# Performance work log

Hardware: AMD Instinct MI355X
Metric: run time of the kernel (lower is better)

## Reference

```python
import jax, jax.numpy as jnp
import numpy as np

EMBED_DIM = 1024
BATCH = 4
SEQ = 2048


def setup_inputs() -> dict:
    key = jax.random.key(0)
    ks = jax.random.split(key, 9)
    D = EMBED_DIM
    s = 1.0 / np.sqrt(D)
    inputs = jax.random.normal(ks[0], (BATCH, SEQ, D), dtype=jnp.float32)
    rotation_params = jax.random.normal(ks[1], (D, D), dtype=jnp.float32) * s
    entangle_params = jax.random.normal(ks[2], (D, D), dtype=jnp.float32) * s
    Wq = jax.random.normal(ks[3], (D, D), dtype=jnp.float32) * s
    bq = jax.random.normal(ks[4], (D,), dtype=jnp.float32) * 0.01
    Wk = jax.random.normal(ks[5], (D, D), dtype=jnp.float32) * s
    bk = jax.random.normal(ks[6], (D,), dtype=jnp.float32) * 0.01
    Wv = jax.random.normal(ks[7], (D, D), dtype=jnp.float32) * s
    bv = jax.random.normal(ks[8], (D,), dtype=jnp.float32) * 0.01
    # causal mask: True = masked out (matches torch masked_fill semantics)
    mask = jnp.triu(jnp.ones((SEQ, SEQ), dtype=bool), k=1)
    return {"inputs": inputs, "rotation_params": rotation_params,
            "entangle_params": entangle_params, "Wq": Wq, "bq": bq,
            "Wk": Wk, "bk": bk, "Wv": Wv, "bv": bv, "mask": mask}


def reference(inputs, rotation_params, entangle_params, Wq, bq, Wk, bk, Wv, bv, mask):
    D = inputs.shape[-1]
    # q = Linear(x) @ R^T ; k = Linear(x) @ E^T ; v = Linear(x)
    q = (jnp.einsum('bsd,ed->bse', inputs, Wq) + bq) @ rotation_params.T
    k = (jnp.einsum('bsd,ed->bse', inputs, Wk) + bk) @ entangle_params.T
    v = jnp.einsum('bsd,ed->bse', inputs, Wv) + bv
    scores = jnp.einsum('bqd,bkd->bqk', q, k) / jnp.sqrt(jnp.float32(D))
    scores = jnp.where(mask, jnp.float32(-jnp.inf), scores)
    probs = jax.nn.softmax(scores, axis=-1)  # dropout=0.0 -> identity
    return jnp.einsum('bqk,bkd->bqd', probs, v)
```

## Files before the change

### kernel.cpp

```cpp
#include <hip/hip_runtime.h>
#include <hip/hip_bf16.h>
#include <stdint.h>
#include <math.h>

#define DD 1024
#define SS 2048
#define BB 4

typedef __bf16 bf16;
typedef __bf16 bf16x8 __attribute__((ext_vector_type(8)));
typedef __bf16 bf16x4 __attribute__((ext_vector_type(4)));
typedef float f32x4 __attribute__((ext_vector_type(4)));

__device__ __forceinline__ void gload_lds16(const bf16* g, bf16* l) {
  __builtin_amdgcn_global_load_lds(
      (const __attribute__((address_space(1))) void*)g,
      (__attribute__((address_space(3))) void*)l, 16, 0, 0);
}

__global__ __launch_bounds__(256) void prep_all(
    const float* __restrict__ x, const float* __restrict__ R,
    const float* __restrict__ E, const float* __restrict__ Wv,
    const float* __restrict__ Wq, const float* __restrict__ Wk,
    const float* __restrict__ bq, const float* __restrict__ bk,
    const float* __restrict__ bv, bf16* __restrict__ xb,
    bf16* __restrict__ Rb, bf16* __restrict__ Eb, bf16* __restrict__ Wvb,
    bf16* __restrict__ WqT, bf16* __restrict__ WkT, float* __restrict__ bias,
    float* __restrict__ rowsums) {
  int bid = blockIdx.x;
  int t = threadIdx.x;
  if (bid < 11264) {
    const float* src;
    bf16* dst;
    int base;
    if (bid < 8192) { src = x; dst = xb; base = bid; }
    else if (bid < 9216) { src = R; dst = Rb; base = bid - 8192; }
    else if (bid < 10240) { src = E; dst = Eb; base = bid - 9216; }
    else { src = Wv; dst = Wvb; base = bid - 10240; }
    int i = (base * 256 + t) * 4;
    float4 v = *(const float4*)(src + i);
    bf16x4 o;
    o.x = (bf16)v.x; o.y = (bf16)v.y; o.z = (bf16)v.z; o.w = (bf16)v.w;
    *(bf16x4*)(dst + i) = o;
  } else if (bid < 13312) {
    int r2 = bid - 11264;
    const float* src = (r2 >= 1024) ? Wk : Wq;
    bf16* dst = (r2 >= 1024) ? WkT : WqT;
    int rem = r2 & 1023;
    int bx = rem & 31, by = rem >> 5;
    __shared__ float tile[32][33];
    int tx = t & 31, ty = t >> 5;
    int xcol = bx * 32 + tx;
    int y0 = by * 32;
    for (int r = ty; r < 32; r += 8)
      tile[r][tx] = src[(y0 + r) * DD + xcol];
    __syncthreads();
    int dx = by * 32 + tx;
    int dy0 = bx * 32;
    for (int r = ty; r < 32; r += 8)
      dst[(dy0 + r) * DD + dx] = (bf16)tile[tx][r];
  } else if (bid < 16384) {
    int e = bid - 13312;
    if (e >= 2048) { if (t == 0) bias[e] = bv[e - 2048]; return; }
    const float* M = (e < 1024) ? R : E;
    const float* bb = (e < 1024) ? bq : bk;
    int row = e & 1023;
    float s = 0.f;
    for (int f = t; f < DD; f += 256) s += M[row * DD + f] * bb[f];
    for (int o = 32; o >= 1; o >>= 1) s += __shfl_xor(s, o, 64);
    __shared__ float red[4];
    if ((t & 63) == 0) red[t >> 6] = s;
    __syncthreads();
    if (t == 0) bias[e] = red[0] + red[1] + red[2] + red[3];
  } else {
    int idx = (bid - 16384) * 256 + t;
    rowsums[idx] = 0.f;
  }
}

#define STGA(p, h, kt)                                                       \
  gload_lds16(A + (long)((h) * 128 + w * 16 + srow) * DD + (kt) * 32 + scg,  \
              As + (p) * 8192 + (h) * 4096 + w * 512)
#define STGB(p, h, kt)                                                       \
  gload_lds16(B + (long)((h) * 128 + w * 16 + srow) * DD + (kt) * 32 + scg,  \
              Bs + (p) * 8192 + (h) * 4096 + w * 512)

#define PHASE(p, q, WAITN, ...)                                              \
  {                                                                          \
    bf16x8 af[4];                                                            \
    _Pragma("unroll") for (int i_ = 0; i_ < 4; i_++)                         \
        af[i_] = *(const bf16x8*)(a_base + (p) * 8192 + (q) * 2048 +         \
                                  i_ * 512);                                 \
    if ((q) == 0) {                                                          \
      _Pragma("unroll") for (int j_ = 0; j_ < 4; j_++)                       \
          bfr[j_] = *(const bf16x8*)(b_base + (p) * 8192 + j_ * 512);        \
    }                                                                        \
    __VA_ARGS__;                                                             \
    __builtin_amdgcn_s_barrier();                                            \
    asm volatile("s_waitcnt lgkmcnt(0)" ::: "memory");                       \
    __builtin_amdgcn_sched_barrier(0);                                       \
    __builtin_amdgcn_s_setprio(1);                                           \
    _Pragma("unroll") for (int i_ = 0; i_ < 4; i_++)                         \
        _Pragma("unroll") for (int j_ = 0; j_ < 4; j_++) acc[(q)*4 + i_][j_] \
        = __builtin_amdgcn_mfma_f32_16x16x32_bf16(af[i_], bfr[j_],           \
                                                  acc[(q)*4 + i_][j_], 0, 0, \
                                                  0);                        \
    __builtin_amdgcn_s_setprio(0);                                           \
    __builtin_amdgcn_sched_barrier(0);                                       \
    if ((WAITN) == 2) asm volatile("s_waitcnt vmcnt(2)" ::: "memory");       \
    if ((WAITN) == 0) asm volatile("s_waitcnt vmcnt(0)" ::: "memory");       \
    __builtin_amdgcn_s_barrier();                                            \
    __builtin_amdgcn_sched_barrier(0);                                       \
  }

__global__ __launch_bounds__(512, 2) void gemm256_qkv(
    const bf16* __restrict__ Ag, const bf16* __restrict__ Bg,
    bf16* __restrict__ Cg, const float* __restrict__ bias,
    bf16* __restrict__ vTp) {
  __shared__ __align__(16) bf16 smem[32768];
  bf16* As = smem;
  bf16* Bs = smem + 16384;

  int id = (int)blockIdx.y * 12 + (int)blockIdx.x;
  int wg = (id & 7) * 48 + (id >> 3);
  int bx = wg % 12, by = wg / 12;
  long m0 = (long)by * 256, n0 = (long)bx * 256;
  const bf16* A = Ag + m0 * DD;
  const bf16* B = Bg + n0 * DD;

  int t = threadIdx.x;
  int w = t >> 6, l = t & 63;
  int wm = w >> 2, wn = w & 3;
  int ln = l & 15, quad = l >> 4;

  int srow = l >> 2;
  int scg = ((l & 3) ^ ((l >> 3) & 3)) * 8;
  int rdslot = (quad ^ ((ln >> 1) & 3)) * 8;
  const bf16* a_base = As + (wm * 128 + ln) * 32 + rdslot;
  const bf16* b_base = Bs + (wn * 64 + ln) * 32 + rdslot;

  f32x4 acc[8][4];
#pragma unroll
  for (int i = 0; i < 8; i++)
#pragma unroll
    for (int j = 0; j < 4; j++) acc[i][j] = f32x4{0.f, 0.f, 0.f, 0.f};
  bf16x8 bfr[4];

  STGA(0, 0, 0); STGA(0, 1, 0);
  STGB(0, 0, 0); STGB(0, 1, 0);
  STGB(1, 0, 1); STGB(1, 1, 1);
  asm volatile("s_waitcnt vmcnt(2)" ::: "memory");
  __builtin_amdgcn_s_barrier();
  __builtin_amdgcn_sched_barrier(0);

#pragma unroll 1
  for (int t2 = 0; t2 < 30; t2 += 2) {
    PHASE(0, 0, -1, { STGA(1, 0, t2 + 1); STGA(1, 1, t2 + 1); })
    PHASE(0, 1, 2, { STGB(0, 0, t2 + 2); STGB(0, 1, t2 + 2); })
    PHASE(1, 0, -1, { STGA(0, 0, t2 + 2); STGA(0, 1, t2 + 2); })
    PHASE(1, 1, 2, { STGB(1, 0, t2 + 3); STGB(1, 1, t2 + 3); })
  }
  PHASE(0, 0, -1, { STGA(1, 0, 31); STGA(1, 1, 31); })
  PHASE(0, 1, 0, {})
  PHASE(1, 0, -1, {})
  PHASE(1, 1, -1, {})

  if (n0 < 2048) {
    bf16* C = Cg + m0 * 3072 + n0;
#pragma unroll
    for (int mf = 0; mf < 8; mf++) {
      int rb = wm * 128 + mf * 16 + quad * 4;
#pragma unroll
      for (int nf = 0; nf < 4; nf++) {
        int col = wn * 64 + nf * 16 + ln;
        float bv_ = bias[n0 + col];
#pragma unroll
        for (int r = 0; r < 4; r++)
          C[(long)(rb + r) * 3072 + col] = (bf16)(acc[mf][nf][r] + bv_);
      }
    }
  } else {
    int d0 = (int)n0 - 2048;
    int b = (int)(m0 >> 11);
    int s0 = (int)(m0 & 2047);
    for (int h = 0; h < 2; ++h) {
      __syncthreads();
      if (wm == h) {
#pragma unroll
        for (int mf = 0; mf < 8; mf++) {
          int sl = mf * 16 + quad * 4;
#pragma unroll
          for (int nf = 0; nf < 4; nf++) {
            int d = wn * 64 + nf * 16 + ln;
            float bv_ = bias[n0 + d];
#pragma unroll
            for (int r = 0; r < 4; r++)
              smem[d * 128 + ((sl + r) ^ ((d & 7) << 3))] =
                  (bf16)(acc[mf][nf][r] + bv_);
          }
        }
      }
      __syncthreads();
      int d = t >> 1, sh = t & 1;
      bf16* dst = vTp + (long)b * DD * SS + (long)(d0 + d) * SS + s0 +
                  h * 128 + sh * 64;
#pragma unroll
      for (int c = 0; c < 8; ++c) {
        int sc = (sh * 64 + c * 8) ^ ((d & 7) << 3);
        *(bf16x8*)(dst + c * 8) = *(const bf16x8*)(smem + d * 128 + sc);
      }
    }
  }
}

template <int MODE>
__global__ __launch_bounds__(256, 4)
void gemm_bt(const bf16* __restrict__ Ag, long lda, long sAb,
             const bf16* __restrict__ Bg, long ldb, long sBb,
             void* __restrict__ Cg, long ldc, long sCb,
             const float* __restrict__ bias, float scale, int K,
             bf16* __restrict__ vTp, float* __restrict__ rowsums) {
  __shared__ __align__(16) bf16 smem[16384];
  bf16* As = smem;
  bf16* Bs = smem + 8192;

  int bx = blockIdx.x, by = blockIdx.y, bz = blockIdx.z;
  if (MODE == 0 || MODE == 1) {
    int nx = (int)gridDim.x;
    int nwg = nx * (int)gridDim.y;
    int id = by * nx + bx;
    int xcd = id & 7, rest = id >> 3;
    int q8 = nwg >> 3, r8 = nwg & 7;
    int wg = (xcd < r8 ? xcd * (q8 + 1) : r8 * (q8 + 1) + (xcd - r8) * q8)
             + rest;
    bx = wg % nx;
    by = wg / nx;
  }
  if (MODE == 1) {
    int q = bx;
    by = (int)((sqrtf(8.f * q + 1.f) - 1.f) * 0.5f);
    while ((by + 1) * (by + 2) / 2 <= q) by++;
    while (by * (by + 1) / 2 > q) by--;
    bx = q - by * (by + 1) / 2;
  }
  if (MODE == 2) by = 15 - by;
  long m0 = (long)by * 128, n0 = (long)bx * 128;
  const bf16* A = Ag + (long)bz * sAb + m0 * lda;
  const bf16* Bp = Bg + (long)bz * sBb + n0 * ldb;

  int t = threadIdx.x;
  int w = t >> 6, l = t & 63;
  int lr = l >> 2;
  int lc = (((l & 3) ^ (lr & 3)) * 8);
  int quad = l >> 4, ln = l & 15;
  int wm = w >> 1, wn = w & 1;
  int rdoff = ((quad ^ (ln & 3)) * 8);

  int Keff = (MODE == 2) ? (by + 1) * 128 : K;

  f32x4 acc[4][4];
#pragma unroll
  for (int i = 0; i < 4; i++)
#pragma unroll
    for (int j = 0; j < 4; j++) acc[i][j] = f32x4{0.f, 0.f, 0.f, 0.f};

  const bf16* a_base = As + (wm * 64 + ln) * 32 + rdoff;
  const bf16* b_base = Bs + (wn * 64 + ln) * 32 + rdoff;
  long arow0 = (long)(w * 16 + lr);

#define STG(p, kc0)                                                         \
  {                                                                         \
    int kc = (kc0) + lc;                                                    \
    gload_lds16(A + arow0 * lda + kc, As + (p) * 4096 + w * 512);           \
    gload_lds16(A + (arow0 + 64) * lda + kc,                                \
                As + (p) * 4096 + 2048 + w * 512);                          \
    gload_lds16(Bp + arow0 * ldb + kc, Bs + (p) * 4096 + w * 512);          \
    gload_lds16(Bp + (arow0 + 64) * ldb + kc,                               \
                Bs + (p) * 4096 + 2048 + w * 512);                          \
  }

  STG(0, 0);
  int cur = 0;
  for (int k = 0; k < Keff; k += 32) {
    asm volatile("s_waitcnt vmcnt(0)" ::: "memory");
    __builtin_amdgcn_s_barrier();
    __builtin_amdgcn_sched_barrier(0);
    if (k + 32 < Keff) STG(cur ^ 1, k + 32);
    bf16x8 af[4], bfr[4];
#pragma unroll
    for (int i = 0; i < 4; i++) {
      af[i] = *(const bf16x8*)(a_base + cur * 4096 + i * 512);
      bfr[i] = *(const bf16x8*)(b_base + cur * 4096 + i * 512);
    }
#pragma unroll
    for (int i = 0; i < 4; i++)
#pragma unroll
      for (int j = 0; j < 4; j++)
        acc[i][j] = __builtin_amdgcn_mfma_f32_16x16x32_bf16(
            af[i], bfr[j], acc[i][j], 0, 0, 0);
    cur ^= 1;
  }
#undef STG
  __syncthreads();

  if (MODE == 0) {
    bf16* C = (bf16*)Cg + (long)bz * sCb + m0 * ldc + n0;
#pragma unroll
    for (int i = 0; i < 4; i++) {
      int rb = wm * 64 + i * 16 + quad * 4;
#pragma unroll
      for (int j = 0; j < 4; j++) {
        int col = wn * 64 + j * 16 + ln;
        float bv_ = bias ? bias[n0 + col] : 0.f;
#pragma unroll
        for (int r = 0; r < 4; r++)
          C[(long)(rb + r) * ldc + col] = (bf16)(acc[i][j][r] + bv_);
      }
    }
  } else if (MODE == 1) {
#pragma unroll
    for (int i = 0; i < 4; i++) {
      int rb = wm * 64 + i * 16 + quad * 4;
#pragma unroll
      for (int j = 0; j < 4; j++) {
        int col = wn * 64 + j * 16 + ln;
#pragma unroll
        for (int r = 0; r < 4; r++) {
          int row = rb + r;
          float p = 0.f;
          if (n0 + col <= m0 + row) p = __expf(acc[i][j][r] * scale);
          smem[row * 128 + (col ^ ((row & 15) << 3))] = (bf16)p;
        }
      }
    }
    __syncthreads();
    int row = t >> 1, h = t & 1;
    bf16* P = (bf16*)Cg + (long)bz * sCb + (m0 + row) * ldc + n0;
    float rsum = 0.f;
#pragma unroll
    for (int jj = 0; jj < 8; jj++) {
      int p8 = h * 8 + jj;
      int slot = p8 ^ (row & 15);
      bf16x8 v = *(const bf16x8*)(smem + row * 128 + slot * 8);
#pragma unroll
      for (int e = 0; e < 8; e++) rsum += (float)v[e];
      *(bf16x8*)(P + p8 * 8) = v;
    }
    atomicAdd(&rowsums[(long)bz * SS + m0 + row], rsum);
  } else {
    float* C = (float*)Cg + (long)bz * sCb + m0 * ldc + n0;
    const float* rs = rowsums + (long)bz * SS + m0;
#pragma unroll
    for (int i = 0; i < 4; i++) {
      int rb = wm * 64 + i * 16 + quad * 4;
      float inv[4];
#pragma unroll
      for (int r = 0; r < 4; r++) inv[r] = 1.f / rs[rb + r];
#pragma unroll
      for (int j = 0; j < 4; j++) {
        int col = wn * 64 + j * 16 + ln;
#pragma unroll
        for (int r = 0; r < 4; r++)
          C[(long)(rb + r) * ldc + col] = acc[i][j][r] * inv[r];
      }
    }
  }
}

extern "C" void kernel_launch(void* const* d_in, const int* in_sizes, int n_in,
                              void* d_out, int out_size, void* d_ws,
                              size_t ws_size, hipStream_t stream) {
  const float* x = (const float*)d_in[0];
  const float* R = (const float*)d_in[1];
  const float* E = (const float*)d_in[2];
  const float* Wq = (const float*)d_in[3];
  const float* bq = (const float*)d_in[4];
  const float* Wk = (const float*)d_in[5];
  const float* bk = (const float*)d_in[6];
  const float* Wv = (const float*)d_in[7];
  const float* bv = (const float*)d_in[8];
  float* out = (float*)d_out;

  char* ws = (char*)d_ws;
  bf16* qkv = (bf16*)ws;
  bf16* vT = (bf16*)(ws + 50331648);
  bf16* probs = (bf16*)(ws + 67108864);
  float* rowsums = (float*)(ws + 100663296);
  char* sr = ws + 101711872;
  bf16* xb = (bf16*)sr;
  bf16* Rb = (bf16*)(sr + 16777216);
  bf16* Eb = Rb + 1024 * 1024;
  bf16* WqT = (bf16*)(sr + 20971520);
  bf16* WkT = WqT + 1024 * 1024;
  bf16* wcat = (bf16*)(sr + 25165824);
  float* bias = (float*)(sr + 31457280);

  prep_all<<<16416, 256, 0, stream>>>(x, R, E, Wv, Wq, Wk, bq, bk, bv, xb, Rb,
                                      Eb, wcat + 2048 * DD, WqT, WkT, bias,
                                      rowsums);

  gemm_bt<0><<<dim3(8, 8, 2), 256, 0, stream>>>(
      Rb, DD, 1024 * 1024, WqT, DD, 1024 * 1024, wcat, DD, 1024 * 1024,
      nullptr, 1.f, DD, nullptr, nullptr);

  gemm256_qkv<<<dim3(12, 32, 1), 512, 0, stream>>>(xb, wcat, qkv, bias, vT);

  gemm_bt<1><<<dim3(136, 1, BB), 256, 0, stream>>>(
      qkv, 3072, (long)SS * 3072, qkv + 1024, 3072, (long)SS * 3072, probs,
      SS, (long)SS * SS, nullptr, 0.03125f, DD, nullptr, rowsums);

  gemm_bt<2><<<dim3(8, 16, BB), 256, 0, stream>>>(
      probs, SS, (long)SS * SS, vT, SS, (long)DD * SS, out,
      DD, (long)SS * DD, nullptr, 1.f, SS, nullptr, rowsums);
}
```

Baseline: 294.3 us.

## Shrink QKV GEMM tile to 128x256 with triple-buffered B and remapped grid

The QKV projection GEMM now uses 128x256 output tiles instead of 256x256, doubling the grid to 768 workgroups. B gets three LDS buffers and A two, on a six-step rotation, and the launch bound asks for 4 waves per SIMD. A new workgroup-to-tile mapping groups tiles into chunks for L2 locality, and the V-transpose epilogue is simplified to one pass. The aim is better occupancy and wave balance across CUs, at the cost of lower arithmetic intensity per tile and more redundant loads of B.

```diff
diff --git a/kernel.cpp b/kernel.cpp
--- a/kernel.cpp
+++ b/kernel.cpp
@@ -78,33 +78,30 @@
   }
 }
 
-#define STGA(p, h, kt)                                                       \
-  gload_lds16(A + (long)((h) * 128 + w * 16 + srow) * DD + (kt) * 32 + scg,  \
-              As + (p) * 8192 + (h) * 4096 + w * 512)
-#define STGB(p, h, kt)                                                       \
+#define QSTGA(pa, kt)                                                        \
+  gload_lds16(A + (long)(w * 16 + srow) * DD + (kt) * 32 + scg,              \
+              As + (pa) * 4096 + w * 512)
+#define QSTGB(pb, h, kt)                                                     \
   gload_lds16(B + (long)((h) * 128 + w * 16 + srow) * DD + (kt) * 32 + scg,  \
-              Bs + (p) * 8192 + (h) * 4096 + w * 512)
-
-#define PHASE(p, q, WAITN, ...)                                              \
+              Bs + (pb) * 8192 + (h) * 4096 + w * 512)
+
+#define QTILE(pa, pb, pa1, pb2, kA, kB, DOA, DOB, WAITN)                     \
   {                                                                          \
-    bf16x8 af[4];                                                            \
+    bf16x8 af[4], bfr[4];                                                    \
     _Pragma("unroll") for (int i_ = 0; i_ < 4; i_++)                         \
-        af[i_] = *(const bf16x8*)(a_base + (p) * 8192 + (q) * 2048 +         \
-                                  i_ * 512);                                 \
-    if ((q) == 0) {                                                          \
-      _Pragma("unroll") for (int j_ = 0; j_ < 4; j_++)                       \
-          bfr[j_] = *(const bf16x8*)(b_base + (p) * 8192 + j_ * 512);        \
-    }                                                                        \
-    __VA_ARGS__;                                                             \
+        af[i_] = *(const bf16x8*)(a_base + (pa) * 4096 + i_ * 512);          \
+    _Pragma("unroll") for (int j_ = 0; j_ < 4; j_++)                         \
+        bfr[j_] = *(const bf16x8*)(b_base + (pb) * 8192 + j_ * 512);         \
+    if (DOA) { QSTGA(pa1, kA); }                                             \
+    if (DOB) { QSTGB(pb2, 0, kB); QSTGB(pb2, 1, kB); }                       \
     __builtin_amdgcn_s_barrier();                                            \
     asm volatile("s_waitcnt lgkmcnt(0)" ::: "memory");                       \
     __builtin_amdgcn_sched_barrier(0);                                       \
     __builtin_amdgcn_s_setprio(1);                                           \
     _Pragma("unroll") for (int i_ = 0; i_ < 4; i_++)                         \
-        _Pragma("unroll") for (int j_ = 0; j_ < 4; j_++) acc[(q)*4 + i_][j_] \
-        = __builtin_amdgcn_mfma_f32_16x16x32_bf16(af[i_], bfr[j_],           \
-                                                  acc[(q)*4 + i_][j_], 0, 0, \
-                                                  0);                        \
+        _Pragma("unroll") for (int j_ = 0; j_ < 4; j_++) acc[i_][j_] =       \
+        __builtin_amdgcn_mfma_f32_16x16x32_bf16(af[i_], bfr[j_],             \
+                                                acc[i_][j_], 0, 0, 0);       \
     __builtin_amdgcn_s_setprio(0);                                           \
     __builtin_amdgcn_sched_barrier(0);                                       \
     if ((WAITN) == 2) asm volatile("s_waitcnt vmcnt(2)" ::: "memory");       \
@@ -113,18 +110,20 @@
     __builtin_amdgcn_sched_barrier(0);                                       \
   }
 
-__global__ __launch_bounds__(512, 2) void gemm256_qkv(
+__global__ __launch_bounds__(512, 4) void gemm_qkv(
     const bf16* __restrict__ Ag, const bf16* __restrict__ Bg,
     bf16* __restrict__ Cg, const float* __restrict__ bias,
     bf16* __restrict__ vTp) {
   __shared__ __align__(16) bf16 smem[32768];
   bf16* As = smem;
-  bf16* Bs = smem + 16384;
+  bf16* Bs = smem + 8192;
 
   int id = (int)blockIdx.y * 12 + (int)blockIdx.x;
-  int wg = (id & 7) * 48 + (id >> 3);
-  int bx = wg % 12, by = wg / 12;
-  long m0 = (long)by * 256, n0 = (long)bx * 256;
+  int wg = (id & 7) * 96 + (id >> 3);
+  int ck = wg / 96, r96 = wg % 96;
+  int bx = (ck & 3) * 3 + r96 % 3;
+  int by = (ck >> 2) * 32 + r96 / 3;
+  long m0 = (long)by * 128, n0 = (long)bx * 256;
   const bf16* A = Ag + m0 * DD;
   const bf16* B = Bg + n0 * DD;
 
@@ -136,79 +135,74 @@
   int srow = l >> 2;
   int scg = ((l & 3) ^ ((l >> 3) & 3)) * 8;
   int rdslot = (quad ^ ((ln >> 1) & 3)) * 8;
-  const bf16* a_base = As + (wm * 128 + ln) * 32 + rdslot;
+  const bf16* a_base = As + (wm * 64 + ln) * 32 + rdslot;
   const bf16* b_base = Bs + (wn * 64 + ln) * 32 + rdslot;
 
-  f32x4 acc[8][4];
-#pragma unroll
-  for (int i = 0; i < 8; i++)
+  f32x4 acc[4][4];
+#pragma unroll
+  for (int i = 0; i < 4; i++)
 #pragma unroll
     for (int j = 0; j < 4; j++) acc[i][j] = f32x4{0.f, 0.f, 0.f, 0.f};
-  bf16x8 bfr[4];
-
-  STGA(0, 0, 0); STGA(0, 1, 0);
-  STGB(0, 0, 0); STGB(0, 1, 0);
-  STGB(1, 0, 1); STGB(1, 1, 1);
+
+  QSTGA(0, 0);
+  QSTGB(0, 0, 0); QSTGB(0, 1, 0);
+  QSTGB(1, 0, 1); QSTGB(1, 1, 1);
   asm volatile("s_waitcnt vmcnt(2)" ::: "memory");
   __builtin_amdgcn_s_barrier();
   __builtin_amdgcn_sched_barrier(0);
 
 #pragma unroll 1
-  for (int t2 = 0; t2 < 30; t2 += 2) {
-    PHASE(0, 0, -1, { STGA(1, 0, t2 + 1); STGA(1, 1, t2 + 1); })
-    PHASE(0, 1, 2, { STGB(0, 0, t2 + 2); STGB(0, 1, t2 + 2); })
-    PHASE(1, 0, -1, { STGA(0, 0, t2 + 2); STGA(0, 1, t2 + 2); })
-    PHASE(1, 1, 2, { STGB(1, 0, t2 + 3); STGB(1, 1, t2 + 3); })
-  }
-  PHASE(0, 0, -1, { STGA(1, 0, 31); STGA(1, 1, 31); })
-  PHASE(0, 1, 0, {})
-  PHASE(1, 0, -1, {})
-  PHASE(1, 1, -1, {})
+  for (int t6 = 0; t6 < 30; t6 += 6) {
+    QTILE(0, 0, 1, 2, t6 + 1, t6 + 2, 1, 1, 2)
+    QTILE(1, 1, 0, 0, t6 + 2, t6 + 3, 1, 1, 2)
+    QTILE(0, 2, 1, 1, t6 + 3, t6 + 4, 1, 1, 2)
+    QTILE(1, 0, 0, 2, t6 + 4, t6 + 5, 1, 1, 2)
+    QTILE(0, 1, 1, 0, t6 + 5, t6 + 6, 1, 1, 2)
+    QTILE(1, 2, 0, 1, t6 + 6, t6 + 7, 1, 1, 2)
+  }
+  QTILE(0, 0, 1, 0, 31, 0, 1, 0, 0)
+  QTILE(1, 1, 0, 0, 0, 0, 0, 0, -1)
+
+  __syncthreads();
 
   if (n0 < 2048) {
     bf16* C = Cg + m0 * 3072 + n0;
 #pragma unroll
-    for (int mf = 0; mf < 8; mf++) {
-      int rb = wm * 128 + mf * 16 + quad * 4;
-#pragma unroll
-      for (int nf = 0; nf < 4; nf++) {
-        int col = wn * 64 + nf * 16 + ln;
+    for (int i = 0; i < 4; i++) {
+      int rb = wm * 64 + i * 16 + quad * 4;
+#pragma unroll
+      for (int j = 0; j < 4; j++) {
+        int col = wn * 64 + j * 16 + ln;
         float bv_ = bias[n0 + col];
 #pragma unroll
         for (int r = 0; r < 4; r++)
-          C[(long)(rb + r) * 3072 + col] = (bf16)(acc[mf][nf][r] + bv_);
+          C[(long)(rb + r) * 3072 + col] = (bf16)(acc[i][j][r] + bv_);
       }
     }
   } else {
     int d0 = (int)n0 - 2048;
     int b = (int)(m0 >> 11);
     int s0 = (int)(m0 & 2047);
-    for (int h = 0; h < 2; ++h) {
-      __syncthreads();
-      if (wm == h) {
-#pragma unroll
-        for (int mf = 0; mf < 8; mf++) {
-          int sl = mf * 16 + quad * 4;
-#pragma unroll
-          for (int nf = 0; nf < 4; nf++) {
-            int d = wn * 64 + nf * 16 + ln;
-            float bv_ = bias[n0 + d];
-#pragma unroll
-            for (int r = 0; r < 4; r++)
-              smem[d * 128 + ((sl + r) ^ ((d & 7) << 3))] =
-                  (bf16)(acc[mf][nf][r] + bv_);
-          }
-        }
+#pragma unroll
+    for (int i = 0; i < 4; i++) {
+      int sl = wm * 64 + i * 16 + quad * 4;
+#pragma unroll
+      for (int j = 0; j < 4; j++) {
+        int d = wn * 64 + j * 16 + ln;
+        float bv_ = bias[n0 + d];
+#pragma unroll
+        for (int r = 0; r < 4; r++)
+          smem[d * 128 + ((sl + r) ^ ((d & 7) << 3))] =
+              (bf16)(acc[i][j][r] + bv_);
       }
-      __syncthreads();
-      int d = t >> 1, sh = t & 1;
-      bf16* dst = vTp + (long)b * DD * SS + (long)(d0 + d) * SS + s0 +
-                  h * 128 + sh * 64;
-#pragma unroll
-      for (int c = 0; c < 8; ++c) {
-        int sc = (sh * 64 + c * 8) ^ ((d & 7) << 3);
-        *(bf16x8*)(dst + c * 8) = *(const bf16x8*)(smem + d * 128 + sc);
-      }
+    }
+    __syncthreads();
+    int d = t >> 1, sh = t & 1;
+    bf16* dst = vTp + (long)b * DD * SS + (long)(d0 + d) * SS + s0 + sh * 64;
+#pragma unroll
+    for (int c = 0; c < 8; ++c) {
+      int sc = (sh * 64 + c * 8) ^ ((d & 7) << 3);
+      *(bf16x8*)(dst + c * 8) = *(const bf16x8*)(smem + d * 128 + sc);
     }
   }
 }
@@ -403,7 +397,7 @@
       Rb, DD, 1024 * 1024, WqT, DD, 1024 * 1024, wcat, DD, 1024 * 1024,
       nullptr, 1.f, DD, nullptr, nullptr);
 
-  gemm256_qkv<<<dim3(12, 32, 1), 512, 0, stream>>>(xb, wcat, qkv, bias, vT);
+  gemm_qkv<<<dim3(12, 64, 1), 512, 0, stream>>>(xb, wcat, qkv, bias, vT);
 
   gemm_bt<1><<<dim3(136, 1, BB), 256, 0, stream>>>(
       qkv, 3072, (long)SS * 3072, qkv + 1024, 3072, (long)SS * 3072, probs,
```

Result: no change. 293.2 us (-0.4%).
